# Kernel optimization log

Measured on AMD Instinct MI355X. Metric: run time of the kernel, lower is better.

The kernel has to match this reference:

```python
import jax, jax.numpy as jnp
import numpy as np

B, N = 8, 2048
ZD, SD, MLP, DEPTH = 512, 64, 2048, 4


def setup_inputs() -> dict:
    key = jax.random.key(0)
    ks = jax.random.split(key, 8)
    g = lambda k, shape: jax.random.normal(k, shape, jnp.float32) * 0.02
    return {
        "z": jax.random.normal(ks[0], (B, N, ZD), jnp.float32),
        "spatial_embedding": jax.random.normal(ks[1], (B, N, SD), jnp.float32) * 0.5,
        "ln_z_scale": jnp.ones((DEPTH, ZD), jnp.float32),
        "ln_z_bias": jnp.zeros((DEPTH, ZD), jnp.float32),
        "ln_s_scale": jnp.ones((DEPTH, ZD), jnp.float32),
        "ln_s_bias": jnp.zeros((DEPTH, ZD), jnp.float32),
        "Wz1": g(ks[2], (DEPTH, ZD, MLP)), "bz1": jnp.zeros((DEPTH, MLP), jnp.float32),
        "Wz2": g(ks[3], (DEPTH, MLP, ZD)), "bz2": jnp.zeros((DEPTH, ZD), jnp.float32),
        "Ws1": g(ks[4], (DEPTH, ZD, MLP)), "bs1": jnp.zeros((DEPTH, MLP), jnp.float32),
        "Ws2": g(ks[5], (DEPTH, MLP, SD)), "bs2": jnp.zeros((DEPTH, SD), jnp.float32),
    }


def _layernorm(x, scale, bias, eps=1e-5):
    m = jnp.mean(x, axis=-1, keepdims=True)
    v = jnp.var(x, axis=-1, keepdims=True)  # biased var, matches torch LayerNorm
    return (x - m) * jax.lax.rsqrt(v + eps) * scale + bias


def _spatial_attn(e, z):
    # sim = exp(-||e_i - e_j||^2), row-normalized == softmax(-d2) over j.
    # Use |a|^2 + |b|^2 - 2ab expansion to avoid the [B,N,N,D] broadcast tensor.
    sq = jnp.sum(e * e, axis=-1)  # [B,N]
    d2 = sq[:, :, None] + sq[:, None, :] - 2.0 * jnp.einsum('bid,bjd->bij', e, e)
    d2 = jnp.maximum(d2, 0.0)
    attn = jax.nn.softmax(-d2, axis=-1)  # [B,N,N]
    return jnp.einsum('bij,bjd->bid', attn, z)


def _ff(x, W1, b1, W2, b2):
    h = jax.nn.gelu(x @ W1 + b1, approximate=False)  # torch nn.GELU() is exact erf
    return h @ W2 + b2


def reference(z, spatial_embedding, ln_z_scale, ln_z_bias, ln_s_scale, ln_s_bias,
              Wz1, bz1, Wz2, bz2, Ws1, bs1, Ws2, bs2):
    s = spatial_embedding
    for i in range(DEPTH):
        z = _spatial_attn(s, z)
        z = _ff(_layernorm(z, ln_z_scale[i], ln_z_bias[i]), Wz1[i], bz1[i], Wz2[i], bz2[i]) + z
        s = _ff(_layernorm(z, ln_s_scale[i], ln_s_bias[i]), Ws1[i], bs1[i], Ws2[i], bs2[i]) + s
    return (z, s)
```

## Files before the change

### kernel.cpp

```cpp
#include <hip/hip_runtime.h>
#include <stdint.h>

#define DEPTH 4
#define BATCH 8
#define NN 2048
#define ZDIM 512
#define SDIM 64
#define MLPD 2048
#define ROWS (BATCH*NN)

typedef __bf16 bf16x8_t __attribute__((ext_vector_type(8)));
typedef float f32x4_t __attribute__((ext_vector_type(4)));
typedef unsigned short us;

#define AS1 __attribute__((address_space(1)))
#define AS3 __attribute__((address_space(3)))

__device__ __forceinline__ void gload16(const void* g, void* l) {
  __builtin_amdgcn_global_load_lds((const AS1 void*)g, (AS3 void*)l, 16, 0, 0);
}

__device__ __forceinline__ unsigned short f2bf(float f) {
  union { float f; unsigned u; } v; v.f = f;
  unsigned u = v.u;
  unsigned r = (u + 0x7fffu + ((u >> 16) & 1u)) >> 16;
  return (unsigned short)r;
}
__device__ __forceinline__ float bf2f(unsigned short h) {
  union { unsigned u; float f; } v; v.u = ((unsigned)h) << 16;
  return v.f;
}

__device__ __forceinline__ float gelu_fast(float x) {
  float x2 = x * x;
  float q = fmaf(x2, -0.0713548162f, -1.5957691216f);
  float em = __expf(q * x);
  return x * __builtin_amdgcn_rcpf(1.0f + em);
}

#define LGKM0() do { asm volatile("s_waitcnt lgkmcnt(0)" ::: "memory"); \
                     __builtin_amdgcn_sched_barrier(0); } while (0)
#define MF(A_, B_, C_) __builtin_amdgcn_mfma_f32_16x16x32_bf16(A_, B_, C_, 0, 0, 0)

__global__ __launch_bounds__(256) void conv_e_kernel(const float* __restrict__ s,
    unsigned short* __restrict__ ebf, float* __restrict__ sq) {
  int lane = threadIdx.x & 63;
  int row = blockIdx.x * 4 + (threadIdx.x >> 6);
  float x = s[(long)row * SDIM + lane];
  unsigned short v = f2bf(x);
  ebf[(long)row * SDIM + lane] = v;
  float xb = bf2f(v);
  float ss = xb * xb;
  #pragma unroll
  for (int off = 32; off > 0; off >>= 1) ss += __shfl_xor(ss, off);
  if (lane == 0) sq[row] = ss;
}

__global__ __launch_bounds__(256) void tconv_kernel(const float* __restrict__ in,
    unsigned short* __restrict__ out, int R, int C, long sIn, long sOut) {
  __shared__ float tile[32][33];
  int b = blockIdx.z;
  int c0 = blockIdx.x * 32, r0 = blockIdx.y * 32;
  int tx = threadIdx.x, ty = threadIdx.y;
  const float* ib = in + (long)b * sIn;
  unsigned short* ob = out + (long)b * sOut;
  #pragma unroll
  for (int i = 0; i < 32; i += 8)
    tile[ty + i][tx] = ib[(long)(r0 + ty + i) * C + c0 + tx];
  __syncthreads();
  #pragma unroll
  for (int i = 0; i < 32; i += 8)
    ob[(long)(c0 + ty + i) * R + r0 + tx] = f2bf(tile[tx][ty + i]);
}

__global__ __launch_bounds__(256) void ln_kernel(const float* __restrict__ x,
    const float* __restrict__ scale, const float* __restrict__ bias,
    unsigned short* __restrict__ y) {
  int lane = threadIdx.x & 63;
  long row = (long)blockIdx.x * 4 + (threadIdx.x >> 6);
  const float* xr = x + row * ZDIM + lane * 8;
  float4 v0 = *(const float4*)xr;
  float4 v1 = *(const float4*)(xr + 4);
  float xv[8] = {v0.x, v0.y, v0.z, v0.w, v1.x, v1.y, v1.z, v1.w};
  float s1 = 0.f, s2 = 0.f;
  #pragma unroll
  for (int k = 0; k < 8; ++k) { s1 += xv[k]; s2 += xv[k] * xv[k]; }
  #pragma unroll
  for (int off = 32; off > 0; off >>= 1) {
    s1 += __shfl_xor(s1, off);
    s2 += __shfl_xor(s2, off);
  }
  float mean = s1 * (1.0f / ZDIM);
  float var = s2 * (1.0f / ZDIM) - mean * mean;
  float rstd = rsqrtf(var + 1e-5f);
  const float* sc = scale + lane * 8;
  const float* bi = bias + lane * 8;
  alignas(16) unsigned short o[8];
  #pragma unroll
  for (int k = 0; k < 8; ++k)
    o[k] = f2bf((xv[k] - mean) * rstd * sc[k] + bi[k]);
  *(uint4*)(y + row * ZDIM + lane * 8) = *(const uint4*)o;
}

__global__ __launch_bounds__(256) void attn_w_kernel(const unsigned short* __restrict__ ebf,
    const float* __restrict__ sq, unsigned short* __restrict__ wout,
    float* __restrict__ RS) {
  __shared__ unsigned short Ei[4096];
  __shared__ unsigned short Ej[8192];
  __shared__ unsigned short Wt[8192];
  int tid = threadIdx.x, lane = tid & 63, wid = tid >> 6;
  int lr = lane & 15, hi = lane >> 4;
  int q = blockIdx.y;
  int b = blockIdx.z;
  int i0 = blockIdx.x * 64;
  const unsigned short* eb = ebf + (long)b * NN * SDIM;

  int rl = tid >> 3;
  int scs = ((tid & 7) ^ (rl & 7)) * 8;
  int dstc = (tid & 192) * 8;

  #pragma unroll
  for (int it = 0; it < 2; ++it)
    gload16(eb + (long)(i0 + it * 32 + rl) * SDIM + scs, &Ei[it * 2048 + dstc]);
  #pragma unroll
  for (int it = 0; it < 4; ++it)
    gload16(eb + (long)(q * 256 + it * 32 + rl) * SDIM + scs, &Ej[it * 2048 + dstc]);
  __syncthreads();

  bf16x8_t afrag[2];
  int ka = lr & 7;
  #pragma unroll
  for (int s = 0; s < 2; ++s)
    afrag[s] = *(const bf16x8_t*)&Ei[(wid * 16 + lr) * 64 + (((s * 4 + hi) ^ ka) * 8)];
  int rloc = wid * 16 + (hi << 2);
  float sqi[4];
  #pragma unroll
  for (int r = 0; r < 4; ++r) sqi[r] = sq[b * NN + i0 + rloc + r];
  float rs[4] = {0.f, 0.f, 0.f, 0.f};
  us* stripe = &Wt[wid * 2048];

  for (int jj = 0; jj < 2; ++jj) {
    int j0 = q * 256 + jj * 128;
    if (jj > 0) {
      __syncthreads();
      #pragma unroll
      for (int it = 0; it < 4; ++it)
        gload16(eb + (long)(j0 + it * 32 + rl) * SDIM + scs, &Ej[it * 2048 + dstc]);
      __syncthreads();
    }
    #pragma unroll
    for (int n = 0; n < 8; ++n) {
      f32x4_t g = {0.f, 0.f, 0.f, 0.f};
      #pragma unroll
      for (int s = 0; s < 2; ++s) {
        int rb = n * 16 + lr;
        bf16x8_t bfr = *(const bf16x8_t*)&Ej[rb * 64 + (((s * 4 + hi) ^ (rb & 7)) * 8)];
        g = __builtin_amdgcn_mfma_f32_16x16x32_bf16(afrag[s], bfr, g, 0, 0, 0);
      }
      float sqj = sq[b * NN + j0 + n * 16 + lr];
      #pragma unroll
      for (int r = 0; r < 4; ++r) {
        float d2 = sqi[r] + sqj - 2.0f * g[r];
        d2 = fmaxf(d2, 0.0f);
        float w = __expf(-d2);
        unsigned short wb = f2bf(w);
        rs[r] += bf2f(wb);
        int srow = (hi << 2) + r;
        stripe[srow * 128 + ((n ^ (srow & 3)) * 16) + lr] = wb;
      }
    }
    LGKM0();
    #pragma unroll
    for (int it = 0; it < 4; ++it) {
      int seg = it * 64 + lane;
      int row = seg >> 4, c8 = seg & 15;
      int c8s = c8 ^ ((row & 3) << 1);
      uint4 v = *(const uint4*)&stripe[row * 128 + c8s * 8];
      long gi = i0 + wid * 16 + row;
      *(uint4*)&wout[(long)b * NN * NN + gi * NN + j0 + c8 * 8] = v;
    }
  }
  #pragma unroll
  for (int off = 1; off < 16; off <<= 1) {
    #pragma unroll
    for (int r = 0; r < 4; ++r) rs[r] += __shfl_xor(rs[r], off);
  }
  if (lr == 0) {
    #pragma unroll
    for (int r = 0; r < 4; ++r)
      RS[(long)q * ROWS + b * NN + i0 + rloc + r] = rs[r];
  }
}

__global__ __launch_bounds__(256, 4) void gemm128ff(
    const unsigned short* __restrict__ A, const unsigned short* __restrict__ BT,
    unsigned short* __restrict__ Cout, const float* __restrict__ bias,
    int Nmat, int K) {
  __shared__ unsigned short LB[16384];
  us* Asb = LB;
  us* Bsb = LB + 8192;
  int tid = threadIdx.x, lane = tid & 63;
  int lr = lane & 15, hi = lane >> 4;
  int wid = tid >> 6, wr = wid >> 1, wc = wid & 1;

  int gx = gridDim.x;
  int wg = blockIdx.y * gx + blockIdx.x;
  int nwg = gx * gridDim.y;
  if ((nwg & 7) == 0) wg = (wg & 7) * (nwg >> 3) + (wg >> 3);
  int bj = wg % gx, bi = wg / gx;
  int row0 = bi * 128, col0 = bj * 128;

  int rl = tid >> 3;
  int scs = ((tid & 7) ^ (rl & 7)) * 8;
  const unsigned short* pA[4];
  const unsigned short* pB[4];
  #pragma unroll
  for (int it = 0; it < 4; ++it) {
    pA[it] = A + (long)(row0 + it * 32 + rl) * K + scs;
    pB[it] = BT + (long)(col0 + it * 32 + rl) * K + scs;
  }
  int dstc = (tid & 192) * 8;

  int offA[4][2], offB[4][2];
  #pragma unroll
  for (int m = 0; m < 4; ++m) {
    #pragma unroll
    for (int s = 0; s < 2; ++s) {
      int ra = wr * 64 + m * 16 + lr;
      offA[m][s] = ra * 64 + (((s * 4 + hi) ^ (ra & 7)) * 8);
      int rb = wc * 64 + m * 16 + lr;
      offB[m][s] = rb * 64 + (((s * 4 + hi) ^ (rb & 7)) * 8);
    }
  }

  auto stage = [&]() {
    #pragma unroll
    for (int it = 0; it < 4; ++it) { gload16(pA[it], &Asb[it * 2048 + dstc]); pA[it] += 64; }
    #pragma unroll
    for (int it = 0; it < 4; ++it) { gload16(pB[it], &Bsb[it * 2048 + dstc]); pB[it] += 64; }
  };

  f32x4_t acc[4][4];
  #pragma unroll
  for (int m = 0; m < 4; ++m)
    #pragma unroll
    for (int n = 0; n < 4; ++n) acc[m][n] = (f32x4_t){0.f, 0.f, 0.f, 0.f};

  int nk = K >> 6;
  stage();

  for (int t = 0; t < nk; ++t) {
    __syncthreads();
    bf16x8_t a0[4], b0[4];
    #pragma unroll
    for (int m = 0; m < 4; ++m) a0[m] = *(const bf16x8_t*)&Asb[offA[m][0]];
    #pragma unroll
    for (int n = 0; n < 4; ++n) b0[n] = *(const bf16x8_t*)&Bsb[offB[n][0]];
    #pragma unroll
    for (int m = 0; m < 4; ++m)
      #pragma unroll
      for (int n = 0; n < 4; ++n)
        acc[m][n] = MF(a0[m], b0[n], acc[m][n]);
    bf16x8_t a1[4], b1[4];
    #pragma unroll
    for (int m = 0; m < 4; ++m) a1[m] = *(const bf16x8_t*)&Asb[offA[m][1]];
    #pragma unroll
    for (int n = 0; n < 4; ++n) b1[n] = *(const bf16x8_t*)&Bsb[offB[n][1]];
    __syncthreads();
    if (t + 1 < nk) stage();
    #pragma unroll
    for (int m = 0; m < 4; ++m)
      #pragma unroll
      for (int n = 0; n < 4; ++n)
        acc[m][n] = MF(a1[m], b1[n], acc[m][n]);
  }

  int cbase = col0 + wc * 64 + lr;
  float bv[4];
  #pragma unroll
  for (int n = 0; n < 4; ++n) bv[n] = bias[cbase + n * 16];
  us* stripe = LB + wid * 4096;
  #pragma unroll
  for (int m = 0; m < 4; ++m) {
    #pragma unroll
    for (int r = 0; r < 4; ++r) {
      int sr = m * 16 + hi * 4 + r;
      #pragma unroll
      for (int n = 0; n < 4; ++n)
        stripe[sr * 64 + ((n ^ (sr & 3)) * 16) + lr] =
            f2bf(gelu_fast(acc[m][n][r] + bv[n]));
    }
  }
  LGKM0();
  #pragma unroll
  for (int it = 0; it < 8; ++it) {
    int seg = it * 64 + lane;
    int sr = seg >> 3, c8 = seg & 7;
    int c8s = c8 ^ ((sr & 3) << 1);
    uint4 v = *(const uint4*)&stripe[sr * 64 + c8s * 8];
    long row = row0 + wr * 64 + sr;
    *(uint4*)&Cout[row * Nmat + col0 + wc * 64 + c8 * 8] = v;
  }
}

template <int EPI>
__global__ __launch_bounds__(256, 4) void gemm128g(
    const unsigned short* __restrict__ A, const unsigned short* __restrict__ BT,
    float* __restrict__ Cout, const float* __restrict__ bias,
    const float* __restrict__ resid, const float* __restrict__ RS,
    int Nmat, int K, long sA, long sB, long sC, long sR) {
  __shared__ unsigned short LB[16384];
  us* Asb = LB;
  us* Bsb = LB + 8192;
  int tid = threadIdx.x, lane = tid & 63;
  int lr = lane & 15, hi = lane >> 4;
  int wid = tid >> 6, wr = wid >> 1, wc = wid & 1;
  int bb = blockIdx.z;

  int gx = gridDim.x;
  int wg = blockIdx.y * gx + blockIdx.x;
  int nwg = gx * gridDim.y;
  if ((nwg & 7) == 0) wg = (wg & 7) * (nwg >> 3) + (wg >> 3);
  int bj = wg % gx, bi = wg / gx;
  int row0 = bi * 128, col0 = bj * 128;

  const unsigned short* Ab = A + (long)bb * sA;
  const unsigned short* Bb = BT + (long)bb * sB;

  int rl = tid >> 3;
  int scs = ((tid & 7) ^ (rl & 7)) * 8;
  const unsigned short* pA[4];
  const unsigned short* pB[4];
  #pragma unroll
  for (int it = 0; it < 4; ++it) {
    pA[it] = Ab + (long)(row0 + it * 32 + rl) * K + scs;
    pB[it] = Bb + (long)(col0 + it * 32 + rl) * K + scs;
  }
  int dstc = (tid & 192) * 8;

  int offA[4][2], offB[4][2];
  #pragma unroll
  for (int m = 0; m < 4; ++m) {
    #pragma unroll
    for (int s = 0; s < 2; ++s) {
      int ra = wr * 64 + m * 16 + lr;
      offA[m][s] = ra * 64 + (((s * 4 + hi) ^ (ra & 7)) * 8);
      int rb = wc * 64 + m * 16 + lr;
      offB[m][s] = rb * 64 + (((s * 4 + hi) ^ (rb & 7)) * 8);
    }
  }

  auto stage = [&]() {
    #pragma unroll
    for (int it = 0; it < 4; ++it) { gload16(pA[it], &Asb[it * 2048 + dstc]); pA[it] += 64; }
    #pragma unroll
    for (int it = 0; it < 4; ++it) { gload16(pB[it], &Bsb[it * 2048 + dstc]); pB[it] += 64; }
  };

  f32x4_t acc[4][4];
  #pragma unroll
  for (int m = 0; m < 4; ++m)
    #pragma unroll
    for (int n = 0; n < 4; ++n) acc[m][n] = (f32x4_t){0.f, 0.f, 0.f, 0.f};

  int nk = K >> 6;
  stage();

  for (int t = 0; t < nk; ++t) {
    __syncthreads();
    bf16x8_t a0[4], b0[4];
    #pragma unroll
    for (int m = 0; m < 4; ++m) a0[m] = *(const bf16x8_t*)&Asb[offA[m][0]];
    #pragma unroll
    for (int n = 0; n < 4; ++n) b0[n] = *(const bf16x8_t*)&Bsb[offB[n][0]];
    #pragma unroll
    for (int m = 0; m < 4; ++m)
      #pragma unroll
      for (int n = 0; n < 4; ++n)
        acc[m][n] = MF(a0[m], b0[n], acc[m][n]);
    bf16x8_t a1[4], b1[4];
    #pragma unroll
    for (int m = 0; m < 4; ++m) a1[m] = *(const bf16x8_t*)&Asb[offA[m][1]];
    #pragma unroll
    for (int n = 0; n < 4; ++n) b1[n] = *(const bf16x8_t*)&Bsb[offB[n][1]];
    __syncthreads();
    if (t + 1 < nk) stage();
    #pragma unroll
    for (int m = 0; m < 4; ++m)
      #pragma unroll
      for (int n = 0; n < 4; ++n)
        acc[m][n] = MF(a1[m], b1[n], acc[m][n]);
  }

  int rbase = row0 + wr * 64 + hi * 4;
  int cbase = col0 + wc * 64 + lr;
  float bv[4];
  #pragma unroll
  for (int n = 0; n < 4; ++n) bv[n] = (EPI == 2) ? bias[cbase + n * 16] : 0.f;
  #pragma unroll
  for (int m = 0; m < 4; ++m) {
    #pragma unroll
    for (int r = 0; r < 4; ++r) {
      int row = rbase + m * 16 + r;
      float ir = 0.f;
      if (EPI == 0) {
        long idx = (long)bb * sR + row;
        float den = 0.f;
        #pragma unroll
        for (int qq = 0; qq < 8; ++qq) den += RS[(long)qq * ROWS + idx];
        ir = 1.0f / den;
      }
      #pragma unroll
      for (int n = 0; n < 4; ++n) {
        int col = cbase + n * 16;
        long cidx = (long)bb * sC + (long)row * Nmat + col;
        if (EPI == 0) {
          Cout[cidx] = acc[m][n][r] * ir;
        } else {
          Cout[cidx] = acc[m][n][r] + bv[n] + resid[(long)bb * sR + (long)row * Nmat + col];
        }
      }
    }
  }
}

__global__ __launch_bounds__(256, 4) void ff2s_part(
    const unsigned short* __restrict__ A, const unsigned short* __restrict__ BT,
    float* __restrict__ SPART, int K) {
  __shared__ unsigned short As[128 * 64];
  __shared__ unsigned short Bs[64 * 64];
  int tid = threadIdx.x, lane = tid & 63;
  int lr = lane & 15, hi = lane >> 4;
  int wid = tid >> 6;
  int kz = blockIdx.z;
  int row0 = blockIdx.y * 128;

  int rl = tid >> 3;
  int scs = ((tid & 7) ^ (rl & 7)) * 8;
  long kbase = (long)kz * 512;
  const unsigned short* pA[4];
  #pragma unroll
  for (int it = 0; it < 4; ++it)
    pA[it] = A + (long)(row0 + it * 32 + rl) * K + kbase + scs;
  const unsigned short* pB[2];
  #pragma unroll
  for (int it = 0; it < 2; ++it)
    pB[it] = BT + (long)(it * 32 + rl) * K + kbase + scs;
  int dstc = (tid & 192) * 8;

  int offA[2][2], offB[4][2];
  #pragma unroll
  for (int m = 0; m < 2; ++m)
    #pragma unroll
    for (int s = 0; s < 2; ++s) {
      int ra = wid * 32 + m * 16 + lr;
      offA[m][s] = ra * 64 + (((s * 4 + hi) ^ (ra & 7)) * 8);
    }
  #pragma unroll
  for (int n = 0; n < 4; ++n)
    #pragma unroll
    for (int s = 0; s < 2; ++s) {
      int rb = n * 16 + lr;
      offB[n][s] = rb * 64 + (((s * 4 + hi) ^ (rb & 7)) * 8);
    }

  auto stage = [&]() {
    #pragma unroll
    for (int it = 0; it < 4; ++it) { gload16(pA[it], &As[it * 2048 + dstc]); pA[it] += 64; }
    #pragma unroll
    for (int it = 0; it < 2; ++it) { gload16(pB[it], &Bs[it * 2048 + dstc]); pB[it] += 64; }
  };

  f32x4_t acc[2][4];
  #pragma unroll
  for (int m = 0; m < 2; ++m)
    #pragma unroll
    for (int n = 0; n < 4; ++n) acc[m][n] = (f32x4_t){0.f, 0.f, 0.f, 0.f};

  stage();
  for (int t = 0; t < 8; ++t) {
    __syncthreads();
    bf16x8_t a0s0 = *(const bf16x8_t*)&As[offA[0][0]];
    bf16x8_t a1s0 = *(const bf16x8_t*)&As[offA[1][0]];
    bf16x8_t a0s1 = *(const bf16x8_t*)&As[offA[0][1]];
    bf16x8_t a1s1 = *(const bf16x8_t*)&As[offA[1][1]];
    bf16x8_t b0s0 = *(const bf16x8_t*)&Bs[offB[0][0]];
    bf16x8_t b1s0 = *(const bf16x8_t*)&Bs[offB[1][0]];
    bf16x8_t b2s0 = *(const bf16x8_t*)&Bs[offB[2][0]];
    bf16x8_t b3s0 = *(const bf16x8_t*)&Bs[offB[3][0]];
    bf16x8_t b0s1 = *(const bf16x8_t*)&Bs[offB[0][1]];
    bf16x8_t b1s1 = *(const bf16x8_t*)&Bs[offB[1][1]];
    bf16x8_t b2s1 = *(const bf16x8_t*)&Bs[offB[2][1]];
    bf16x8_t b3s1 = *(const bf16x8_t*)&Bs[offB[3][1]];
    __syncthreads();
    if (t + 1 < 8) stage();
    acc[0][0] = MF(a0s0, b0s0, acc[0][0]);
    acc[1][0] = MF(a1s0, b0s0, acc[1][0]);
    acc[0][1] = MF(a0s0, b1s0, acc[0][1]);
    acc[1][1] = MF(a1s0, b1s0, acc[1][1]);
    acc[0][2] = MF(a0s0, b2s0, acc[0][2]);
    acc[1][2] = MF(a1s0, b2s0, acc[1][2]);
    acc[0][3] = MF(a0s0, b3s0, acc[0][3]);
    acc[1][3] = MF(a1s0, b3s0, acc[1][3]);
    acc[0][0] = MF(a0s1, b0s1, acc[0][0]);
    acc[1][0] = MF(a1s1, b0s1, acc[1][0]);
    acc[0][1] = MF(a0s1, b1s1, acc[0][1]);
    acc[1][1] = MF(a1s1, b1s1, acc[1][1]);
    acc[0][2] = MF(a0s1, b2s1, acc[0][2]);
    acc[1][2] = MF(a1s1, b2s1, acc[1][2]);
    acc[0][3] = MF(a0s1, b3s1, acc[0][3]);
    acc[1][3] = MF(a1s1, b3s1, acc[1][3]);
  }

  float* outp = SPART + (long)kz * ROWS * SDIM;
  #pragma unroll
  for (int m = 0; m < 2; ++m) {
    #pragma unroll
    for (int r = 0; r < 4; ++r) {
      int row = row0 + wid * 32 + m * 16 + hi * 4 + r;
      #pragma unroll
      for (int n = 0; n < 4; ++n)
        outp[(long)row * SDIM + n * 16 + lr] = acc[m][n][r];
    }
  }
}

__global__ __launch_bounds__(256) void ff2s_red(const float* __restrict__ SPART,
    const float* __restrict__ bias, const float* __restrict__ resid,
    float* __restrict__ out) {
  long idx = (long)blockIdx.x * 256 + threadIdx.x;
  int col = idx & (SDIM - 1);
  float v = SPART[idx] + SPART[(long)ROWS * SDIM + idx] +
            SPART[2L * ROWS * SDIM + idx] + SPART[3L * ROWS * SDIM + idx];
  out[idx] = v + bias[col] + resid[idx];
}

extern "C" void kernel_launch(void* const* d_in, const int* in_sizes, int n_in,
                              void* d_out, int out_size, void* d_ws, size_t ws_size,
                              hipStream_t stream) {
  (void)in_sizes; (void)n_in; (void)out_size; (void)ws_size;
  const float* in_z   = (const float*)d_in[0];
  const float* in_s   = (const float*)d_in[1];
  const float* lnz_sc = (const float*)d_in[2];
  const float* lnz_bi = (const float*)d_in[3];
  const float* lns_sc = (const float*)d_in[4];
  const float* lns_bi = (const float*)d_in[5];
  const float* Wz1 = (const float*)d_in[6];
  const float* bz1 = (const float*)d_in[7];
  const float* Wz2 = (const float*)d_in[8];
  const float* bz2 = (const float*)d_in[9];
  const float* Ws1 = (const float*)d_in[10];
  const float* bs1 = (const float*)d_in[11];
  const float* Ws2 = (const float*)d_in[12];
  const float* bs2 = (const float*)d_in[13];
  float* out_z = (float*)d_out;
  float* out_s = out_z + (long)ROWS * ZDIM;

  char* ws = (char*)d_ws;
  size_t off = 0;
  auto alloc = [&](size_t bytes) { void* p = ws + off; off += (bytes + 255) & ~(size_t)255; return p; };
  unsigned short* WH   = (unsigned short*)alloc((size_t)BATCH * NN * NN * 2);
  unsigned short* ZT   = (unsigned short*)alloc((size_t)BATCH * ZDIM * NN * 2);
  unsigned short* XLN  = (unsigned short*)alloc((size_t)ROWS * ZDIM * 2);
  unsigned short* EBF  = (unsigned short*)alloc((size_t)ROWS * SDIM * 2);
  float* ZATT = (float*)alloc((size_t)ROWS * ZDIM * 4);
  float* ZBUF = (float*)alloc((size_t)ROWS * ZDIM * 4);
  float* SBUF = (float*)alloc((size_t)ROWS * SDIM * 4);
  float* SQ   = (float*)alloc((size_t)ROWS * 4);
  float* RS   = (float*)alloc((size_t)8 * ROWS * 4);
  float* SPART = (float*)alloc((size_t)4 * ROWS * SDIM * 4);
  unsigned short* W1Z = (unsigned short*)alloc((size_t)DEPTH * MLPD * ZDIM * 2);
  unsigned short* W2Z = (unsigned short*)alloc((size_t)DEPTH * ZDIM * MLPD * 2);
  unsigned short* W1S = (unsigned short*)alloc((size_t)DEPTH * MLPD * ZDIM * 2);
  unsigned short* W2S = (unsigned short*)alloc((size_t)DEPTH * SDIM * MLPD * 2);

  tconv_kernel<<<dim3(MLPD / 32, ZDIM / 32, DEPTH), dim3(32, 8), 0, stream>>>(
      Wz1, W1Z, ZDIM, MLPD, (long)ZDIM * MLPD, (long)MLPD * ZDIM);
  tconv_kernel<<<dim3(ZDIM / 32, MLPD / 32, DEPTH), dim3(32, 8), 0, stream>>>(
      Wz2, W2Z, MLPD, ZDIM, (long)MLPD * ZDIM, (long)ZDIM * MLPD);
  tconv_kernel<<<dim3(MLPD / 32, ZDIM / 32, DEPTH), dim3(32, 8), 0, stream>>>(
      Ws1, W1S, ZDIM, MLPD, (long)ZDIM * MLPD, (long)MLPD * ZDIM);
  tconv_kernel<<<dim3(SDIM / 32, MLPD / 32, DEPTH), dim3(32, 8), 0, stream>>>(
      Ws2, W2S, MLPD, SDIM, (long)MLPD * SDIM, (long)SDIM * MLPD);

  for (int L = 0; L < DEPTH; ++L) {
    const float* z_in = (L == 0) ? in_z : ZBUF;
    const float* s_in = (L == 0) ? in_s : SBUF;
    float* z_out = (L == DEPTH - 1) ? out_z : ZBUF;
    float* s_out = (L == DEPTH - 1) ? out_s : SBUF;

    conv_e_kernel<<<ROWS / 4, 256, 0, stream>>>(s_in, EBF, SQ);
    tconv_kernel<<<dim3(ZDIM / 32, NN / 32, BATCH), dim3(32, 8), 0, stream>>>(
        z_in, ZT, NN, ZDIM, (long)NN * ZDIM, (long)ZDIM * NN);
    attn_w_kernel<<<dim3(NN / 64, 8, BATCH), 256, 0, stream>>>(EBF, SQ, WH, RS);
    gemm128g<0><<<dim3(ZDIM / 128, NN / 128, BATCH), 256, 0, stream>>>(
        WH, ZT, ZATT, nullptr, nullptr, RS,
        ZDIM, NN, (long)NN * NN, (long)ZDIM * NN, (long)NN * ZDIM, NN);
    ln_kernel<<<ROWS / 4, 256, 0, stream>>>(ZATT, lnz_sc + L * ZDIM, lnz_bi + L * ZDIM, XLN);
    gemm128ff<<<dim3(MLPD / 128, ROWS / 128, 1), 256, 0, stream>>>(
        XLN, W1Z + (long)L * MLPD * ZDIM, WH, bz1 + L * MLPD, MLPD, ZDIM);
    gemm128g<2><<<dim3(ZDIM / 128, ROWS / 128, 1), 256, 0, stream>>>(
        WH, W2Z + (long)L * ZDIM * MLPD, z_out, bz2 + L * ZDIM, ZATT, nullptr,
        ZDIM, MLPD, 0, 0, 0, 0);
    ln_kernel<<<ROWS / 4, 256, 0, stream>>>(z_out, lns_sc + L * ZDIM, lns_bi + L * ZDIM, XLN);
    gemm128ff<<<dim3(MLPD / 128, ROWS / 128, 1), 256, 0, stream>>>(
        XLN, W1S + (long)L * MLPD * ZDIM, WH, bs1 + L * MLPD, MLPD, ZDIM);
    ff2s_part<<<dim3(1, ROWS / 128, 4), 256, 0, stream>>>(
        WH, W2S + (long)L * SDIM * MLPD, SPART, MLPD);
    ff2s_red<<<ROWS * SDIM / 256, 256, 0, stream>>>(
        SPART, bs2 + L * SDIM, s_in, s_out);
  }
}
```

Before: 942.6 us.

## Replace 128x128 4-wave FF1 GEMM with single-wave 64x64 double-buffered kernel

```diff
diff --git a/kernel.cpp b/kernel.cpp
--- a/kernel.cpp
+++ b/kernel.cpp
@@ -192,53 +192,50 @@
   }
 }
 
-__global__ __launch_bounds__(256, 4) void gemm128ff(
+__global__ __launch_bounds__(64) void gemm1w2(
     const unsigned short* __restrict__ A, const unsigned short* __restrict__ BT,
     unsigned short* __restrict__ Cout, const float* __restrict__ bias,
     int Nmat, int K) {
-  __shared__ unsigned short LB[16384];
-  us* Asb = LB;
-  us* Bsb = LB + 8192;
-  int tid = threadIdx.x, lane = tid & 63;
+  __shared__ unsigned short As[2][2048];
+  __shared__ unsigned short Bs[2][2048];
+  int lane = threadIdx.x & 63;
   int lr = lane & 15, hi = lane >> 4;
-  int wid = tid >> 6, wr = wid >> 1, wc = wid & 1;
 
   int gx = gridDim.x;
   int wg = blockIdx.y * gx + blockIdx.x;
   int nwg = gx * gridDim.y;
   if ((nwg & 7) == 0) wg = (wg & 7) * (nwg >> 3) + (wg >> 3);
   int bj = wg % gx, bi = wg / gx;
-  int row0 = bi * 128, col0 = bj * 128;
-
-  int rl = tid >> 3;
-  int scs = ((tid & 7) ^ (rl & 7)) * 8;
+  int row0 = bi * 64, col0 = bj * 64;
+
+  int r4 = lane >> 2;
+  int c4 = lane & 3;
   const unsigned short* pA[4];
   const unsigned short* pB[4];
   #pragma unroll
   for (int it = 0; it < 4; ++it) {
-    pA[it] = A + (long)(row0 + it * 32 + rl) * K + scs;
-    pB[it] = BT + (long)(col0 + it * 32 + rl) * K + scs;
-  }
-  int dstc = (tid & 192) * 8;
-
-  int offA[4][2], offB[4][2];
+    int row = it * 16 + r4;
+    int sc = (c4 ^ ((row >> 1) & 3)) * 8;
+    pA[it] = A + (long)(row0 + row) * K + sc;
+    pB[it] = BT + (long)(col0 + row) * K + sc;
+  }
+
+  auto stage = [&](int buf) {
+    #pragma unroll
+    for (int it = 0; it < 4; ++it) {
+      gload16(pA[it], &As[buf][it * 512]);
+      gload16(pB[it], &Bs[buf][it * 512]);
+      pA[it] += 32;
+      pB[it] += 32;
+    }
+  };
+
+  int offs[4];
   #pragma unroll
   for (int m = 0; m < 4; ++m) {
-    #pragma unroll
-    for (int s = 0; s < 2; ++s) {
-      int ra = wr * 64 + m * 16 + lr;
-      offA[m][s] = ra * 64 + (((s * 4 + hi) ^ (ra & 7)) * 8);
-      int rb = wc * 64 + m * 16 + lr;
-      offB[m][s] = rb * 64 + (((s * 4 + hi) ^ (rb & 7)) * 8);
-    }
-  }
-
-  auto stage = [&]() {
-    #pragma unroll
-    for (int it = 0; it < 4; ++it) { gload16(pA[it], &Asb[it * 2048 + dstc]); pA[it] += 64; }
-    #pragma unroll
-    for (int it = 0; it < 4; ++it) { gload16(pB[it], &Bsb[it * 2048 + dstc]); pB[it] += 64; }
-  };
+    int row = m * 16 + lr;
+    offs[m] = row * 32 + ((hi ^ ((row >> 1) & 3)) * 8);
+  }
 
   f32x4_t acc[4][4];
   #pragma unroll
@@ -246,40 +243,36 @@
     #pragma unroll
     for (int n = 0; n < 4; ++n) acc[m][n] = (f32x4_t){0.f, 0.f, 0.f, 0.f};
 
-  int nk = K >> 6;
-  stage();
+  int nk = K >> 5;
+  stage(0);
 
   for (int t = 0; t < nk; ++t) {
-    __syncthreads();
-    bf16x8_t a0[4], b0[4];
-    #pragma unroll
-    for (int m = 0; m < 4; ++m) a0[m] = *(const bf16x8_t*)&Asb[offA[m][0]];
-    #pragma unroll
-    for (int n = 0; n < 4; ++n) b0[n] = *(const bf16x8_t*)&Bsb[offB[n][0]];
+    int cur = t & 1;
+    if (t + 1 < nk) {
+      stage(cur ^ 1);
+      asm volatile("s_waitcnt vmcnt(8)" ::: "memory");
+    } else {
+      asm volatile("s_waitcnt vmcnt(0)" ::: "memory");
+    }
+    bf16x8_t a[4], b[4];
+    #pragma unroll
+    for (int m = 0; m < 4; ++m) a[m] = *(const bf16x8_t*)&As[cur][offs[m]];
+    #pragma unroll
+    for (int n = 0; n < 4; ++n) b[n] = *(const bf16x8_t*)&Bs[cur][offs[n]];
+    asm volatile("s_waitcnt lgkmcnt(0)" ::: "memory");
+    __builtin_amdgcn_sched_barrier(0);
     #pragma unroll
     for (int m = 0; m < 4; ++m)
       #pragma unroll
       for (int n = 0; n < 4; ++n)
-        acc[m][n] = MF(a0[m], b0[n], acc[m][n]);
-    bf16x8_t a1[4], b1[4];
-    #pragma unroll
-    for (int m = 0; m < 4; ++m) a1[m] = *(const bf16x8_t*)&Asb[offA[m][1]];
-    #pragma unroll
-    for (int n = 0; n < 4; ++n) b1[n] = *(const bf16x8_t*)&Bsb[offB[n][1]];
-    __syncthreads();
-    if (t + 1 < nk) stage();
-    #pragma unroll
-    for (int m = 0; m < 4; ++m)
-      #pragma unroll
-      for (int n = 0; n < 4; ++n)
-        acc[m][n] = MF(a1[m], b1[n], acc[m][n]);
-  }
-
-  int cbase = col0 + wc * 64 + lr;
+        acc[m][n] = MF(a[m], b[n], acc[m][n]);
+  }
+
+  int cbase = col0 + lr;
   float bv[4];
   #pragma unroll
   for (int n = 0; n < 4; ++n) bv[n] = bias[cbase + n * 16];
-  us* stripe = LB + wid * 4096;
+  us* stripe = &As[0][0];
   #pragma unroll
   for (int m = 0; m < 4; ++m) {
     #pragma unroll
@@ -298,8 +291,8 @@
     int sr = seg >> 3, c8 = seg & 7;
     int c8s = c8 ^ ((sr & 3) << 1);
     uint4 v = *(const uint4*)&stripe[sr * 64 + c8s * 8];
-    long row = row0 + wr * 64 + sr;
-    *(uint4*)&Cout[row * Nmat + col0 + wc * 64 + c8 * 8] = v;
+    long row = row0 + sr;
+    *(uint4*)&Cout[row * Nmat + col0 + c8 * 8] = v;
   }
 }
 
@@ -597,13 +590,13 @@
         WH, ZT, ZATT, nullptr, nullptr, RS,
         ZDIM, NN, (long)NN * NN, (long)ZDIM * NN, (long)NN * ZDIM, NN);
     ln_kernel<<<ROWS / 4, 256, 0, stream>>>(ZATT, lnz_sc + L * ZDIM, lnz_bi + L * ZDIM, XLN);
-    gemm128ff<<<dim3(MLPD / 128, ROWS / 128, 1), 256, 0, stream>>>(
+    gemm1w2<<<dim3(MLPD / 64, ROWS / 64, 1), 64, 0, stream>>>(
         XLN, W1Z + (long)L * MLPD * ZDIM, WH, bz1 + L * MLPD, MLPD, ZDIM);
     gemm128g<2><<<dim3(ZDIM / 128, ROWS / 128, 1), 256, 0, stream>>>(
         WH, W2Z + (long)L * ZDIM * MLPD, z_out, bz2 + L * ZDIM, ZATT, nullptr,
         ZDIM, MLPD, 0, 0, 0, 0);
     ln_kernel<<<ROWS / 4, 256, 0, stream>>>(z_out, lns_sc + L * ZDIM, lns_bi + L * ZDIM, XLN);
-    gemm128ff<<<dim3(MLPD / 128, ROWS / 128, 1), 256, 0, stream>>>(
+    gemm1w2<<<dim3(MLPD / 64, ROWS / 64, 1), 64, 0, stream>>>(
         XLN, W1S + (long)L * MLPD * ZDIM, WH, bs1 + L * MLPD, MLPD, ZDIM);
     ff2s_part<<<dim3(1, ROWS / 128, 4), 256, 0, stream>>>(
         WH, W2S + (long)L * SDIM * MLPD, SPART, MLPD);
```

Result: slower. 1.166 ms (+23.7%).
